# Optimization experiments

Measured on AMD Instinct MI355X. Metric: run time of the kernel, lower is better.

The kernel has to match this reference:

```python
import jax, jax.numpy as jnp
import numpy as np

D_IN = 3
HID = 256
N_BRANCH = 8
SKIP_IN = (4,)
CSG_TREE = [0, 1, [2, 3], [4, 5, [6, 7]]]
FLAG_CONVEX = True
BETA = 100.0
N_POINTS = 100000

# layer dims: [3, 256*7, 8]; layer whose OUTPUT feeds a skip layer emits 256-3=253
_DIMS = [D_IN] + [HID] * 7 + [N_BRANCH]


def _layer_out_dim(layer):
    if (layer + 1) in SKIP_IN:
        return _DIMS[layer + 1] - D_IN
    return _DIMS[layer + 1]


def setup_inputs() -> dict:
    key = jax.random.key(0)
    keys = jax.random.split(key, 20)
    inp = {"x": jax.random.normal(keys[0], (N_POINTS, D_IN), dtype=jnp.float32)}
    n_layers = len(_DIMS) - 1  # 8 linear layers
    for layer in range(n_layers):
        in_d = _DIMS[layer]
        out_d = _layer_out_dim(layer)
        kw = jax.random.fold_in(keys[1], layer)
        if layer == n_layers - 1:  # geometric init of last layer
            W = (np.sqrt(np.pi) / np.sqrt(in_d)
                 + 1e-5 * jax.random.normal(kw, (in_d, out_d), dtype=jnp.float32))
            b = -1.0 * jnp.ones((out_d,), dtype=jnp.float32)
        else:
            W = (np.sqrt(2.0) / np.sqrt(out_d)) * jax.random.normal(
                kw, (in_d, out_d), dtype=jnp.float32)
            b = jnp.zeros((out_d,), dtype=jnp.float32)
        inp[f"W{layer}"] = W
        inp[f"b{layer}"] = b
    return inp


def _softplus_beta(x):
    return jax.nn.softplus(BETA * x) / BETA


def _csg_combine(vals, ops, cvx_flag):
    # hard CSG tree: one-hot matmul == column gather; recursion is static (trace time)
    idxs = [v for v in ops if not isinstance(v, list)]
    cols = [vals[:, jnp.array(idxs)]]
    for v in ops:
        if isinstance(v, list):
            cols.append(_csg_combine(vals, v, not cvx_flag))
    m = jnp.concatenate(cols, axis=1)
    red = jnp.max if cvx_flag else jnp.min
    return red(m, axis=1, keepdims=True)


def _forward(x, Ws, bs):
    inp = x
    h = x
    n_layers = len(Ws)
    inv_sqrt2 = np.float32(1.0 / np.sqrt(2.0))
    for layer in range(n_layers):
        if layer in SKIP_IN:
            h = jnp.concatenate([h, inp], axis=-1) * inv_sqrt2
        h = h @ Ws[layer] + bs[layer]
        if layer < n_layers - 1:
            h = _softplus_beta(h)
    branch_vals = h  # [N, n_branch]
    hcsg = _csg_combine(branch_vals, CSG_TREE, FLAG_CONVEX)  # [N, 1]
    return jnp.concatenate([hcsg, branch_vals], axis=1)  # flag_output == 0


def reference(x, W0, b0, W1, b1, W2, b2, W3, b3, W4, b4, W5, b5, W6, b6, W7, b7):
    Ws = [W0, W1, W2, W3, W4, W5, W6, W7]
    bs = [b0, b1, b2, b3, b4, b5, b6, b7]
    return _forward(x, Ws, bs)
```

## Files before the change

kernel.cpp:

```cpp
#include <hip/hip_runtime.h>
#include <hip/hip_bf16.h>


using bf16x8 = __attribute__((ext_vector_type(8))) __bf16;
using f32x4  = __attribute__((ext_vector_type(4))) float;

#define LDA 264

#define OFFW0 0
#define OFFW1 8192
#define OFFW7 401408
#define WSB_BYTE_OFF 811008
#define OFFB7 1792

#define SCALE_T2 144.26950408889634f
#define INV_SQRT2 0.70710678118654752f
#define LN2_100 0.0069314718055994531f

__device__ __forceinline__ float fast_exp2(float x) {
#if __has_builtin(__builtin_amdgcn_exp2f)
    return __builtin_amdgcn_exp2f(x);
#else
    return exp2f(x);
#endif
}
__device__ __forceinline__ float fast_log2(float x) {
#if __has_builtin(__builtin_amdgcn_logf)
    return __builtin_amdgcn_logf(x);
#else
    return log2f(x);
#endif
}

__device__ __forceinline__ float softplus_t2(float t2) {
    float e = fast_exp2(-fabsf(t2));
    float l = fast_log2(1.0f + e);
    return fmaxf(t2, 0.0f) + l;
}

__device__ __forceinline__ unsigned short bf16_rne(float f) {
    unsigned int u = __float_as_uint(f);
    unsigned int r = u + 0x7FFFu + ((u >> 16) & 1u);
    return (unsigned short)(r >> 16);
}

template <int KK, int NTG>
__device__ __forceinline__ void mfma_group(
    const unsigned short* __restrict__ wfrag,
    const float* __restrict__ bias,
    const unsigned short* act,
    f32x4 (&acc)[2][NTG], int wave, int lane)
{
    const int quad = lane >> 4;
    const int l15  = lane & 15;

#pragma unroll
    for (int i = 0; i < 2; ++i) {
        const int chb = (wave * 2 + i) * 16 + quad * 4;
        const float4 b4 = *(const float4*)(bias + chb);
#pragma unroll
        for (int nt = 0; nt < NTG; ++nt)
            acc[i][nt] = f32x4{b4.x, b4.y, b4.z, b4.w};
    }

    const unsigned short* wbase = wfrag + (wave * 2 * KK * 64 + lane) * 8;

#pragma unroll
    for (int kk = 0; kk < KK; ++kk) {
        bf16x8 bfr[NTG];
#pragma unroll
        for (int nt = 0; nt < NTG; ++nt)
            bfr[nt] = *(const bf16x8*)(act + (nt * 16 + l15) * LDA + kk * 32 + quad * 8);
#pragma unroll
        for (int i = 0; i < 2; ++i) {
            bf16x8 afr = *(const bf16x8*)(wbase + (i * KK + kk) * 512);
#pragma unroll
            for (int nt = 0; nt < NTG; ++nt)
                acc[i][nt] = __builtin_amdgcn_mfma_f32_16x16x32_bf16(afr, bfr[nt], acc[i][nt], 0, 0, 0);
        }
    }
}

template <int NTG>
__device__ __forceinline__ void epi_group(
    f32x4 (&acc)[2][NTG], unsigned short* act, const float* xst,
    int wave, int lane, bool splice)
{
    const int quad = lane >> 4;
    const int l15  = lane & 15;

#pragma unroll
    for (int i = 0; i < 2; ++i) {
        const int chb = (wave * 2 + i) * 16 + quad * 4;
#pragma unroll
        for (int nt = 0; nt < NTG; ++nt) {
            const int pt = nt * 16 + l15;
            float vv[4];
#pragma unroll
            for (int r = 0; r < 4; ++r)
                vv[r] = softplus_t2(acc[i][nt][r]);
            if (splice && chb == 252) {
                vv[1] = xst[pt * 4 + 0];
                vv[2] = xst[pt * 4 + 1];
                vv[3] = xst[pt * 4 + 2];
            }
            __hip_bfloat162 p01 = __float22bfloat162_rn(float2{vv[0], vv[1]});
            __hip_bfloat162 p23 = __float22bfloat162_rn(float2{vv[2], vv[3]});
            uint2 pk;
            pk.x = *(unsigned int*)&p01;
            pk.y = *(unsigned int*)&p23;
            *(uint2*)(act + pt * LDA + chb) = pk;
        }
    }
}

template <int NTG>
__device__ __forceinline__ void run_net(
    const float* __restrict__ x, float* __restrict__ out,
    const unsigned short* __restrict__ wsW, const float* __restrict__ wsB,
    unsigned short* act, float* xst,
    int base_pt, int npts, int tid)
{
    const int wave = tid >> 6, lane = tid & 63;
    const int quad = lane >> 4, l15 = lane & 15;

    for (int i = tid; i < 2 * NTG * 16 * 32; i += 512) {
        const int pt = i >> 5, ch = i & 31;
        const int ptg = base_pt + pt;
        float v = 0.0f;
        if (ch < 3 && ptg < npts) v = x[ptg * 3 + ch];
        act[pt * LDA + ch] = bf16_rne(v);
        if (ch < 4) xst[pt * 4 + ch] = (ch < 3) ? v : 0.0f;
    }
    __syncthreads();

    unsigned short* actA = act;
    unsigned short* actB = act + NTG * 16 * LDA;
    const float* xstA = xst;
    const float* xstB = xst + NTG * 16 * 4;

    f32x4 accA[2][NTG], accB[2][NTG];

    mfma_group<1, NTG>(wsW + OFFW0, wsB, actA, accA, wave, lane);
    __syncthreads();

    mfma_group<1, NTG>(wsW + OFFW0, wsB, actB, accB, wave, lane);
    epi_group<NTG>(accA, actA, xstA, wave, lane, false);
    __syncthreads();

#pragma unroll 1
    for (int l = 1; l <= 6; ++l) {
        const unsigned short* Wl = wsW + OFFW1 + (l - 1) * 65536;
        const float* bl = wsB + l * 256;

        mfma_group<8, NTG>(Wl, bl, actA, accA, wave, lane);
        epi_group<NTG>(accB, actB, xstB, wave, lane, l == 4);
        __syncthreads();

        mfma_group<8, NTG>(Wl, bl, actB, accB, wave, lane);
        epi_group<NTG>(accA, actA, xstA, wave, lane, l == 3);
        __syncthreads();
    }

    epi_group<NTG>(accB, actB, xstB, wave, lane, false);
    __syncthreads();

    if (wave < 2 * NTG) {
        const float4 b4 = *(const float4*)(wsB + OFFB7 + quad * 4);
        f32x4 acc = f32x4{b4.x, b4.y, b4.z, b4.w};
        const unsigned short* w7 = wsW + OFFW7;
#pragma unroll
        for (int kk = 0; kk < 8; ++kk) {
            bf16x8 bfr = *(const bf16x8*)(act + (wave * 16 + l15) * LDA + kk * 32 + quad * 8);
            bf16x8 afr = *(const bf16x8*)(w7 + (kk * 64 + lane) * 8);
            acc = __builtin_amdgcn_mfma_f32_16x16x32_bf16(afr, bfr, acc, 0, 0, 0);
        }
        float u0 = __shfl(acc[0], l15 + 16);
        float u1 = __shfl(acc[1], l15 + 16);
        float u2 = __shfl(acc[2], l15 + 16);
        float u3 = __shfl(acc[3], l15 + 16);
        if (quad == 0) {
            const int ptg = base_pt + wave * 16 + l15;
            if (ptg < npts) {
                const float v0 = acc[0], v1 = acc[1], v2 = acc[2], v3 = acc[3];
                const float v4 = u0, v5 = u1, v6 = u2, v7 = u3;
                const float m23   = fminf(v2, v3);
                const float m67   = fmaxf(v6, v7);
                const float m4567 = fminf(fminf(v4, v5), m67);
                const float h     = fmaxf(fmaxf(v0, v1), fmaxf(m23, m4567));
                float* o = out + (long)ptg * 9;
                o[0] = h;
                o[1] = v0; o[2] = v1; o[3] = v2; o[4] = v3;
                o[5] = v4; o[6] = v5; o[7] = v6; o[8] = v7;
            }
        }
    }
}

__global__ __launch_bounds__(512, 4)
void nhrep_main(const float* __restrict__ x, float* __restrict__ out,
                const unsigned short* __restrict__ wsW,
                const float* __restrict__ wsB, int npts, int nbig)
{
    __shared__ unsigned short act[96 * LDA];
    __shared__ float xst[96 * 4];
    const int b = blockIdx.x;
    if (b < nbig) {
        run_net<3>(x, out, wsW, wsB, act, xst, b * 96, npts, threadIdx.x);
    } else {
        run_net<1>(x, out, wsW, wsB, act, xst,
                   nbig * 96 + (b - nbig) * 32, npts, threadIdx.x);
    }
}

struct PackArgs {
    const float* W[8];
    const float* b[8];
};

#define TOTAL_FRAGS 50688
#define TOTAL_BIAS  1808

__global__ void prepack_all(PackArgs args, unsigned short* __restrict__ dstW,
                            float* __restrict__ dstB)
{
    const int t = blockIdx.x * blockDim.x + threadIdx.x;
    const int FB[9]  = {0, 1024, 9216, 17408, 25600, 33792, 41984, 50176, 50688};
    const int KKs[8] = {1, 8, 8, 8, 8, 8, 8, 8};
    const int ind[8] = {3, 256, 256, 256, 256, 256, 256, 256};
    const int outd[8]= {256, 256, 256, 253, 256, 256, 256, 8};

    if (t < TOTAL_FRAGS) {
        int l = 0;
        while (t >= FB[l + 1]) ++l;
        const int f    = t - FB[l];
        const int lane = f & 63;
        const int kk   = (f >> 6) % KKs[l];
        const int mt   = f / (64 * KKs[l]);
        const int o    = mt * 16 + (lane & 15);
        const int kb   = kk * 32 + (lane >> 4) * 8;
        const float* W = args.W[l];
        const int in_d = ind[l], out_d = outd[l];

        unsigned short v[8];
#pragma unroll
        for (int j = 0; j < 8; ++j) {
            const int k = kb + j;
            float w = 0.0f;
            if (k < in_d && o < out_d) {
                float sc = 1.0f;
                if (l == 0) sc = SCALE_T2;
                else if (l == 4) sc = (k < 253) ? INV_SQRT2 : (SCALE_T2 * INV_SQRT2);
                else if (l == 7) sc = LN2_100;
                w = W[k * out_d + o] * sc;
            }
            unsigned int u = __float_as_uint(w);
            v[j] = (unsigned short)((u + 0x7FFFu + ((u >> 16) & 1u)) >> 16);
        }
        uint4 p;
        p.x = (unsigned int)v[0] | ((unsigned int)v[1] << 16);
        p.y = (unsigned int)v[2] | ((unsigned int)v[3] << 16);
        p.z = (unsigned int)v[4] | ((unsigned int)v[5] << 16);
        p.w = (unsigned int)v[6] | ((unsigned int)v[7] << 16);
        *(uint4*)(dstW + (long)t * 8) = p;
    } else if (t < TOTAL_FRAGS + TOTAL_BIAS) {
        const int u = t - TOTAL_FRAGS;
        const int l = (u < 1792) ? (u >> 8) : 7;
        const int idx = (l < 7) ? (u & 255) : (u - 1792);
        const float sc = (l < 7) ? SCALE_T2 : 1.0f;
        dstB[u] = (idx < outd[l]) ? args.b[l][idx] * sc : 0.0f;
    }
}

extern "C" void kernel_launch(void* const* d_in, const int* in_sizes, int n_in,
                              void* d_out, int out_size, void* d_ws, size_t ws_size,
                              hipStream_t stream)
{
    const float* x = (const float*)d_in[0];
    unsigned short* wsW = (unsigned short*)d_ws;
    float* wsB = (float*)((char*)d_ws + WSB_BYTE_OFF);

    PackArgs pa;
    for (int l = 0; l < 8; ++l) {
        pa.W[l] = (const float*)d_in[1 + 2 * l];
        pa.b[l] = (const float*)d_in[2 + 2 * l];
    }
    const int ptot = TOTAL_FRAGS + TOTAL_BIAS;
    prepack_all<<<(ptot + 255) / 256, 256, 0, stream>>>(pa, wsW, wsB);

    const int npts = in_sizes[0] / 3;
    int nbig, nsmall;
    const int tail_pts = 16384;
    if (npts > tail_pts) {
        nbig = (npts - tail_pts + 95) / 96;
        const int base_small = nbig * 96;
        nsmall = (npts - base_small + 31) / 32;
    } else {
        nbig = 0;
        nsmall = (npts + 31) / 32;
    }
    nhrep_main<<<nbig + nsmall, 512, 0, stream>>>(x, (float*)d_out, wsW, wsB,
                                                  npts, nbig);
}
```

Measured before the change: 194.9 us.

## Interleave softplus epilogue into MFMA k-loop and shrink big tiles to 64 points

The per-layer MFMA pass and the previous half-tile's softplus epilogue are fused into one staggered loop, so epilogue work for one accumulator slice is issued between the MFMA batches of each k-step. The final layer-7 projection for the A half is started before the B-half epilogue to overlap the tail. Big blocks go from 96 to 64 points (NTG 3 to 2), reducing LDS and register use and increasing block count. An unused, broken epi_group stub is left behind, and smaller tiles reuse each weight fragment across fewer points.

```diff
diff --git a/kernel.cpp b/kernel.cpp
--- a/kernel.cpp
+++ b/kernel.cpp
@@ -81,6 +81,30 @@
     }
 }
 
+template <int I, int NT>
+__device__ __forceinline__ void epi_slice(
+    const f32x4& a4, unsigned short* act, const float* xst,
+    bool splice, int wave, int quad, int l15)
+{
+    const int chb = (wave * 2 + I) * 16 + quad * 4;
+    const int pt  = NT * 16 + l15;
+    float vv[4];
+#pragma unroll
+    for (int r = 0; r < 4; ++r)
+        vv[r] = softplus_t2(a4[r]);
+    if (splice && chb == 252) {
+        vv[1] = xst[pt * 4 + 0];
+        vv[2] = xst[pt * 4 + 1];
+        vv[3] = xst[pt * 4 + 2];
+    }
+    __hip_bfloat162 p01 = __float22bfloat162_rn(float2{vv[0], vv[1]});
+    __hip_bfloat162 p23 = __float22bfloat162_rn(float2{vv[2], vv[3]});
+    uint2 pk;
+    pk.x = *(unsigned int*)&p01;
+    pk.y = *(unsigned int*)&p23;
+    *(uint2*)(act + pt * LDA + chb) = pk;
+}
+
 template <int NTG>
 __device__ __forceinline__ void epi_group(
     f32x4 (&acc)[2][NTG], unsigned short* act, const float* xst,
@@ -88,7 +112,21 @@
 {
     const int quad = lane >> 4;
     const int l15  = lane & 15;
-
+#pragma unroll
+    for (int i = 0; i < 2; ++i)
+#pragma unroll
+        for (int nt = 0; nt < NTG; ++nt) {
+            if (i == 0) epi_slice<0, 0>(acc[0][nt], act + nt * 16 * LDA - 0, xst + nt * 0, splice, wave, quad, l15);
+        }
+}
+
+template <int NTG>
+__device__ __forceinline__ void epi_group_full(
+    f32x4 (&acc)[2][NTG], unsigned short* act, const float* xst,
+    int wave, int lane, bool splice)
+{
+    const int quad = lane >> 4;
+    const int l15  = lane & 15;
 #pragma unroll
     for (int i = 0; i < 2; ++i) {
         const int chb = (wave * 2 + i) * 16 + quad * 4;
@@ -114,6 +152,105 @@
     }
 }
 
+template <int KK, int NTG>
+__device__ __forceinline__ void stag_region(
+    const unsigned short* __restrict__ wfrag,
+    const float* __restrict__ bias,
+    const unsigned short* __restrict__ actX,
+    unsigned short* actY,
+    f32x4 (&accX)[2][NTG], f32x4 (&accY)[2][NTG],
+    const float* xstY, bool splice, int wave, int lane)
+{
+    const int quad = lane >> 4;
+    const int l15  = lane & 15;
+
+#pragma unroll
+    for (int i = 0; i < 2; ++i) {
+        const int chb = (wave * 2 + i) * 16 + quad * 4;
+        const float4 b4 = *(const float4*)(bias + chb);
+#pragma unroll
+        for (int nt = 0; nt < NTG; ++nt)
+            accX[i][nt] = f32x4{b4.x, b4.y, b4.z, b4.w};
+    }
+
+    const unsigned short* wbase = wfrag + (wave * 2 * KK * 64 + lane) * 8;
+
+#pragma unroll
+    for (int kk = 0; kk < KK; ++kk) {
+        bf16x8 bfr[NTG];
+#pragma unroll
+        for (int nt = 0; nt < NTG; ++nt)
+            bfr[nt] = *(const bf16x8*)(actX + (nt * 16 + l15) * LDA + kk * 32 + quad * 8);
+        bf16x8 afr0 = *(const bf16x8*)(wbase + kk * 512);
+        bf16x8 afr1 = *(const bf16x8*)(wbase + (KK + kk) * 512);
+
+        if (kk < 2 * NTG) {
+            constexpr int c = 0;  (void)c;
+            const int i  = kk & 1;
+            const int nt = kk >> 1;
+            const int chb = (wave * 2 + i) * 16 + quad * 4;
+            const int pt  = nt * 16 + l15;
+            float vv[4];
+#pragma unroll
+            for (int r = 0; r < 4; ++r)
+                vv[r] = softplus_t2(accY[i][nt][r]);
+            if (splice && chb == 252) {
+                vv[1] = xstY[pt * 4 + 0];
+                vv[2] = xstY[pt * 4 + 1];
+                vv[3] = xstY[pt * 4 + 2];
+            }
+            __hip_bfloat162 p01 = __float22bfloat162_rn(float2{vv[0], vv[1]});
+            __hip_bfloat162 p23 = __float22bfloat162_rn(float2{vv[2], vv[3]});
+            uint2 pk;
+            pk.x = *(unsigned int*)&p01;
+            pk.y = *(unsigned int*)&p23;
+            *(uint2*)(actY + pt * LDA + chb) = pk;
+        }
+
+#pragma unroll
+        for (int nt = 0; nt < NTG; ++nt)
+            accX[0][nt] = __builtin_amdgcn_mfma_f32_16x16x32_bf16(afr0, bfr[nt], accX[0][nt], 0, 0, 0);
+#pragma unroll
+        for (int nt = 0; nt < NTG; ++nt)
+            accX[1][nt] = __builtin_amdgcn_mfma_f32_16x16x32_bf16(afr1, bfr[nt], accX[1][nt], 0, 0, 0);
+    }
+}
+
+__device__ __forceinline__ void l7_part(
+    const unsigned short* act, const unsigned short* __restrict__ w7,
+    const float* __restrict__ wsB, float* __restrict__ out,
+    int row0, int ptg0, int npts, int lane)
+{
+    const int quad = lane >> 4, l15 = lane & 15;
+    const float4 b4 = *(const float4*)(wsB + OFFB7 + quad * 4);
+    f32x4 acc = f32x4{b4.x, b4.y, b4.z, b4.w};
+#pragma unroll
+    for (int kk = 0; kk < 8; ++kk) {
+        bf16x8 bfr = *(const bf16x8*)(act + (row0 + l15) * LDA + kk * 32 + quad * 8);
+        bf16x8 afr = *(const bf16x8*)(w7 + (kk * 64 + lane) * 8);
+        acc = __builtin_amdgcn_mfma_f32_16x16x32_bf16(afr, bfr, acc, 0, 0, 0);
+    }
+    float u0 = __shfl(acc[0], l15 + 16);
+    float u1 = __shfl(acc[1], l15 + 16);
+    float u2 = __shfl(acc[2], l15 + 16);
+    float u3 = __shfl(acc[3], l15 + 16);
+    if (quad == 0) {
+        const int ptg = ptg0 + l15;
+        if (ptg < npts) {
+            const float v0 = acc[0], v1 = acc[1], v2 = acc[2], v3 = acc[3];
+            const float v4 = u0, v5 = u1, v6 = u2, v7 = u3;
+            const float m23   = fminf(v2, v3);
+            const float m67   = fmaxf(v6, v7);
+            const float m4567 = fminf(fminf(v4, v5), m67);
+            const float h     = fmaxf(fmaxf(v0, v1), fmaxf(m23, m4567));
+            float* o = out + (long)ptg * 9;
+            o[0] = h;
+            o[1] = v0; o[2] = v1; o[3] = v2; o[4] = v3;
+            o[5] = v4; o[6] = v5; o[7] = v6; o[8] = v7;
+        }
+    }
+}
+
 template <int NTG>
 __device__ __forceinline__ void run_net(
     const float* __restrict__ x, float* __restrict__ out,
@@ -122,7 +259,6 @@
     int base_pt, int npts, int tid)
 {
     const int wave = tid >> 6, lane = tid & 63;
-    const int quad = lane >> 4, l15 = lane & 15;
 
     for (int i = tid; i < 2 * NTG * 16 * 32; i += 512) {
         const int pt = i >> 5, ch = i & 31;
@@ -143,9 +279,8 @@
 
     mfma_group<1, NTG>(wsW + OFFW0, wsB, actA, accA, wave, lane);
     __syncthreads();
-
     mfma_group<1, NTG>(wsW + OFFW0, wsB, actB, accB, wave, lane);
-    epi_group<NTG>(accA, actA, xstA, wave, lane, false);
+    epi_group_full<NTG>(accA, actA, xstA, wave, lane, false);
     __syncthreads();
 
 #pragma unroll 1
@@ -153,48 +288,21 @@
         const unsigned short* Wl = wsW + OFFW1 + (l - 1) * 65536;
         const float* bl = wsB + l * 256;
 
-        mfma_group<8, NTG>(Wl, bl, actA, accA, wave, lane);
-        epi_group<NTG>(accB, actB, xstB, wave, lane, l == 4);
+        stag_region<8, NTG>(Wl, bl, actA, actB, accA, accB, xstB, l == 4, wave, lane);
         __syncthreads();
 
-        mfma_group<8, NTG>(Wl, bl, actB, accB, wave, lane);
-        epi_group<NTG>(accA, actA, xstA, wave, lane, l == 3);
+        stag_region<8, NTG>(Wl, bl, actB, actA, accB, accA, xstA, l == 3, wave, lane);
         __syncthreads();
     }
 
-    epi_group<NTG>(accB, actB, xstB, wave, lane, false);
+    if (wave < NTG)
+        l7_part(act, wsW + OFFW7, wsB, out, wave * 16, base_pt + wave * 16, npts, lane);
+    epi_group_full<NTG>(accB, actB, xstB, wave, lane, false);
     __syncthreads();
 
-    if (wave < 2 * NTG) {
-        const float4 b4 = *(const float4*)(wsB + OFFB7 + quad * 4);
-        f32x4 acc = f32x4{b4.x, b4.y, b4.z, b4.w};
-        const unsigned short* w7 = wsW + OFFW7;
-#pragma unroll
-        for (int kk = 0; kk < 8; ++kk) {
-            bf16x8 bfr = *(const bf16x8*)(act + (wave * 16 + l15) * LDA + kk * 32 + quad * 8);
-            bf16x8 afr = *(const bf16x8*)(w7 + (kk * 64 + lane) * 8);
-            acc = __builtin_amdgcn_mfma_f32_16x16x32_bf16(afr, bfr, acc, 0, 0, 0);
-        }
-        float u0 = __shfl(acc[0], l15 + 16);
-        float u1 = __shfl(acc[1], l15 + 16);
-        float u2 = __shfl(acc[2], l15 + 16);
-        float u3 = __shfl(acc[3], l15 + 16);
-        if (quad == 0) {
-            const int ptg = base_pt + wave * 16 + l15;
-            if (ptg < npts) {
-                const float v0 = acc[0], v1 = acc[1], v2 = acc[2], v3 = acc[3];
-                const float v4 = u0, v5 = u1, v6 = u2, v7 = u3;
-                const float m23   = fminf(v2, v3);
-                const float m67   = fmaxf(v6, v7);
-                const float m4567 = fminf(fminf(v4, v5), m67);
-                const float h     = fmaxf(fmaxf(v0, v1), fmaxf(m23, m4567));
-                float* o = out + (long)ptg * 9;
-                o[0] = h;
-                o[1] = v0; o[2] = v1; o[3] = v2; o[4] = v3;
-                o[5] = v4; o[6] = v5; o[7] = v6; o[8] = v7;
-            }
-        }
-    }
+    if (wave < NTG)
+        l7_part(act, wsW + OFFW7, wsB, out,
+                NTG * 16 + wave * 16, base_pt + NTG * 16 + wave * 16, npts, lane);
 }
 
 __global__ __launch_bounds__(512, 4)
@@ -202,14 +310,14 @@
                 const unsigned short* __restrict__ wsW,
                 const float* __restrict__ wsB, int npts, int nbig)
 {
-    __shared__ unsigned short act[96 * LDA];
-    __shared__ float xst[96 * 4];
+    __shared__ unsigned short act[64 * LDA];
+    __shared__ float xst[64 * 4];
     const int b = blockIdx.x;
     if (b < nbig) {
-        run_net<3>(x, out, wsW, wsB, act, xst, b * 96, npts, threadIdx.x);
+        run_net<2>(x, out, wsW, wsB, act, xst, b * 64, npts, threadIdx.x);
     } else {
         run_net<1>(x, out, wsW, wsB, act, xst,
-                   nbig * 96 + (b - nbig) * 32, npts, threadIdx.x);
+                   nbig * 64 + (b - nbig) * 32, npts, threadIdx.x);
     }
 }
 
@@ -292,8 +400,8 @@
     int nbig, nsmall;
     const int tail_pts = 16384;
     if (npts > tail_pts) {
-        nbig = (npts - tail_pts + 95) / 96;
-        const int base_small = nbig * 96;
+        nbig = (npts - tail_pts + 63) / 64;
+        const int base_small = nbig * 64;
         nsmall = (npts - base_small + 31) / 32;
     } else {
         nbig = 0;
```

Measured after the change: 193.3 us. Within noise of the previous version (-0.8%).
